# Performance work log

Measured on AMD Instinct MI355X. Metric: run time of the kernel, lower is better.

The kernel has to match this reference:

```python
import jax, jax.numpy as jnp
import numpy as np

STAGES = [80, 40, 20]
INPUT = 640
NUM_CLASSES = 80
B = 32
PRE_NMS = 1000      # top-k candidates fed to NMS (fixed-shape surrogate for full sort)
MAX_DET = 100       # max_num_detections
IOU_TH = 0.5
CLASS_OFF = 4096.0  # batched_nms trick: offset boxes per class so classes never overlap


def setup_inputs() -> dict:
    key = jax.random.key(0)
    ks = jax.random.split(key, 6)
    inp = {}
    for i, s in enumerate(STAGES):
        inp[f"cls{i}"] = jax.random.normal(ks[2 * i], (B, NUM_CLASSES, s, s), dtype=jnp.float32)
        # positive ltrb distances, up to ~64 px
        inp[f"box{i}"] = jax.random.uniform(ks[2 * i + 1], (B, 4, s, s), dtype=jnp.float32) * 64.0
    return inp


def _decode_level(cls, box, stage):
    # cls: [B,C,H,W], box: [B,4,H,W]
    step = INPUT // stage
    cls = jax.nn.sigmoid(jnp.transpose(cls, (0, 2, 3, 1)))   # [B,H,W,C]
    conf = jnp.max(cls, axis=-1)                             # [B,H,W]
    cidx = jnp.argmax(cls, axis=-1)                          # [B,H,W]
    box = jnp.transpose(box, (0, 2, 3, 1))                   # [B,H,W,4]
    grid = jnp.arange(stage, dtype=box.dtype) * step
    gx, gy = jnp.meshgrid(grid, grid, indexing='xy')
    block = jnp.stack([gx, gy], axis=-1)                     # [H,W,2]
    xy1 = block - box[..., :2]
    xy2 = block + box[..., 2:4]
    boxes = jnp.concatenate([xy1, xy2], axis=-1).reshape(box.shape[0], -1, 4)
    return boxes, conf.reshape(conf.shape[0], -1), cidx.reshape(cidx.shape[0], -1)


def _iou_matrix(b):
    # b: [N,4] -> [N,N] pairwise IoU
    area = jnp.maximum(b[:, 2] - b[:, 0], 0.) * jnp.maximum(b[:, 3] - b[:, 1], 0.)
    lt = jnp.maximum(b[:, None, :2], b[None, :, :2])
    rb = jnp.minimum(b[:, None, 2:], b[None, :, 2:])
    wh = jnp.maximum(rb - lt, 0.)
    inter = wh[..., 0] * wh[..., 1]
    return inter / (area[:, None] + area[None, :] - inter + 1e-7)


def _nms_image(boxes, scores, classes):
    # class-aware (batched) NMS via per-class coordinate offset
    off = classes.astype(boxes.dtype) * CLASS_OFF
    ob = boxes + off[:, None]
    s_top, idx = jax.lax.top_k(scores, PRE_NMS)
    b_top = ob[idx]                                          # [PRE,4], score-sorted desc
    iou = _iou_matrix(b_top)
    ar = jnp.arange(PRE_NMS)

    def body(i, supp):
        row = (iou[i] > IOU_TH) & (ar > i)
        return jnp.where(supp[i], supp, supp | row)

    supp = jax.lax.fori_loop(0, PRE_NMS, body, jnp.zeros((PRE_NMS,), bool))
    kept_scores = jnp.where(supp, -jnp.inf, s_top)
    sel_s, sel = jax.lax.top_k(kept_scores, MAX_DET)
    final = idx[sel]                                         # indices into original 8400
    valid = jnp.isfinite(sel_s)
    out_b = jnp.where(valid[:, None], boxes[final], 0.)
    out_s = jnp.where(valid, scores[final], 0.)
    out_c = jnp.where(valid, classes[final], -1)
    return out_b, out_s, out_c


def reference(cls0, box0, cls1, box1, cls2, box2):
    parts = [_decode_level(c, b, s) for c, b, s in
             zip([cls0, cls1, cls2], [box0, box1, box2], STAGES)]
    boxes = jnp.concatenate([p[0] for p in parts], axis=1)    # [B,8400,4]
    scores = jnp.concatenate([p[1] for p in parts], axis=1)   # [B,8400]
    classes = jnp.concatenate([p[2] for p in parts], axis=1)  # [B,8400]
    ob, os_, oc = jax.vmap(_nms_image)(boxes, scores, classes)
    boxes_with_scores = jnp.concatenate([ob, os_[..., None]], axis=-1)  # [B,MAX_DET,5]
    return boxes_with_scores, oc
```

## Files before the change

kernel.cpp:

```cpp
#include <hip/hip_runtime.h>

typedef unsigned int u32;
typedef unsigned long long u64;

#define NB 32
#define NCLS 80
#define NANCHOR 8400
#define PRE 1000
#define MAXDET 100
#define NT 1024

__global__ void decode_kernel(const float* __restrict__ cls0, const float* __restrict__ box0,
                              const float* __restrict__ cls1, const float* __restrict__ box1,
                              const float* __restrict__ cls2, const float* __restrict__ box2,
                              float* __restrict__ ws_scores, float4* __restrict__ ws_boxes,
                              int* __restrict__ ws_cls) {
    int g = blockIdx.x * blockDim.x + threadIdx.x;
    if (g >= NB * NANCHOR) return;
    int b = g / NANCHOR;
    int r = g - b * NANCHOR;

    const float* cp; const float* bp;
    int HW, hw, h, w, step;
    if (r < 6400) {
        cp = cls0 + (size_t)b * NCLS * 6400; bp = box0 + (size_t)b * 4 * 6400;
        HW = 6400; hw = r;        h = hw / 80; w = hw - h * 80; step = 8;
    } else if (r < 8000) {
        cp = cls1 + (size_t)b * NCLS * 1600; bp = box1 + (size_t)b * 4 * 1600;
        HW = 1600; hw = r - 6400; h = hw / 40; w = hw - h * 40; step = 16;
    } else {
        cp = cls2 + (size_t)b * NCLS * 400;  bp = box2 + (size_t)b * 4 * 400;
        HW = 400;  hw = r - 8000; h = hw / 20; w = hw - h * 20; step = 32;
    }

    float m = cp[hw];
    int ci = 0;
    for (int c = 1; c < NCLS; ++c) {
        float v = cp[(size_t)c * HW + hw];
        if (v > m) { m = v; ci = c; }
    }
    float score = 1.0f / (1.0f + expf(-m));

    float l = bp[hw], t = bp[HW + hw], rr = bp[2 * HW + hw], bo = bp[3 * HW + hw];
    float gx = (float)(w * step), gy = (float)(h * step);

    ws_scores[g] = score;
    ws_boxes[g] = make_float4(gx - l, gy - t, gx + rr, gy + bo);
    ws_cls[g] = ci;
}

__global__ __launch_bounds__(NT) void nms_kernel(const float* __restrict__ ws_scores,
                                                 const float4* __restrict__ ws_boxes,
                                                 const int* __restrict__ ws_cls,
                                                 float* __restrict__ out) {
    const int b = blockIdx.x;
    const int tid = threadIdx.x;

    __shared__ int s_hist[1024];
    __shared__ u64 s_key[2048];
    __shared__ float s_x1[PRE], s_y1[PRE], s_x2[PRE], s_y2[PRE], s_area[PRE];
    __shared__ int s_supp[PRE];
    __shared__ int s_keep[MAXDET];
    __shared__ int s_C, s_base;
    __shared__ u32 s_thresh;
    __shared__ int s_cnt;

    const float* sc = ws_scores + (size_t)b * NANCHOR;

    s_hist[tid] = 0;
    __syncthreads();
    for (int a = tid; a < NANCHOR; a += NT) {
        u32 sb = __float_as_uint(sc[a]);
        atomicAdd(&s_hist[sb >> 20], 1);
    }
    __syncthreads();
    for (int off = 1; off < 1024; off <<= 1) {
        int v = s_hist[tid];
        int u = (tid + off < 1024) ? s_hist[tid + off] : 0;
        __syncthreads();
        s_hist[tid] = v + u;
        __syncthreads();
    }
    {
        int sfx = s_hist[tid];
        int nxt = (tid < 1023) ? s_hist[tid + 1] : 0;
        if (sfx >= PRE && (tid == 1023 || nxt < PRE)) { s_C = tid; s_base = nxt; }
    }
    __syncthreads();
    const int C = s_C, base = s_base;
    __syncthreads();

    s_hist[tid] = 0;
    __syncthreads();
    for (int a = tid; a < NANCHOR; a += NT) {
        u32 sb = __float_as_uint(sc[a]);
        if ((int)(sb >> 20) == C) atomicAdd(&s_hist[(sb >> 10) & 1023], 1);
    }
    __syncthreads();
    for (int off = 1; off < 1024; off <<= 1) {
        int v = s_hist[tid];
        int u = (tid + off < 1024) ? s_hist[tid + off] : 0;
        __syncthreads();
        s_hist[tid] = v + u;
        __syncthreads();
    }
    {
        int sfx = base + s_hist[tid];
        int nxt = base + ((tid < 1023) ? s_hist[tid + 1] : 0);
        if (sfx >= PRE && (tid == 1023 || nxt < PRE))
            s_thresh = ((u32)C << 20) | ((u32)tid << 10);
    }
    if (tid == 0) s_cnt = 0;
    s_key[tid] = 0ULL;
    s_key[tid + 1024] = 0ULL;
    __syncthreads();
    const u32 thresh = s_thresh;

    for (int a = tid; a < NANCHOR; a += NT) {
        u32 sb = __float_as_uint(sc[a]);
        if (sb >= thresh) {
            int pos = atomicAdd(&s_cnt, 1);
            if (pos < 2048)
                s_key[pos] = ((u64)sb << 14) | (u64)(NANCHOR - 1 - a);
        }
    }
    __syncthreads();

    for (int k = 2; k <= 2048; k <<= 1) {
        for (int j = k >> 1; j > 0; j >>= 1) {
            for (int i = tid; i < 2048; i += NT) {
                int ixj = i ^ j;
                if (ixj > i) {
                    u64 va = s_key[i], vb = s_key[ixj];
                    bool desc = ((i & k) == 0);
                    if (desc ? (va < vb) : (va > vb)) { s_key[i] = vb; s_key[ixj] = va; }
                }
            }
            __syncthreads();
        }
    }

    if (tid < PRE) {
        u64 key = s_key[tid];
        int idx = (NANCHOR - 1) - (int)(key & 16383ULL);
        float4 bx = ws_boxes[(size_t)b * NANCHOR + idx];
        int c = ws_cls[(size_t)b * NANCHOR + idx];
        float off = (float)c * 4096.0f;
        float x1 = bx.x + off, y1 = bx.y + off, x2 = bx.z + off, y2 = bx.w + off;
        s_x1[tid] = x1; s_y1[tid] = y1; s_x2[tid] = x2; s_y2[tid] = y2;
        s_area[tid] = fmaxf(x2 - x1, 0.0f) * fmaxf(y2 - y1, 0.0f);
        s_supp[tid] = 0;
    }
    __syncthreads();

    int nkept = 0;
    for (int i = 0; i < PRE; ++i) {
        if (s_supp[i]) continue;
        if (tid == 0) s_keep[nkept] = i;
        nkept++;
        if (nkept >= MAXDET) break;
        float xi1 = s_x1[i], yi1 = s_y1[i], xi2 = s_x2[i], yi2 = s_y2[i], ai = s_area[i];
        int j = i + 1 + tid;
        if (j < PRE && !s_supp[j]) {
            float lx = fmaxf(xi1, s_x1[j]);
            float ly = fmaxf(yi1, s_y1[j]);
            float rx = fminf(xi2, s_x2[j]);
            float ry = fminf(yi2, s_y2[j]);
            float wx = fmaxf(rx - lx, 0.0f);
            float wy = fmaxf(ry - ly, 0.0f);
            float inter = wx * wy;
            float iou = inter / (ai + s_area[j] - inter + 1e-7f);
            if (iou > 0.5f) s_supp[j] = 1;
        }
        __syncthreads();
    }
    __syncthreads();

    if (tid < MAXDET) {
        float* o = out + ((size_t)b * MAXDET + tid) * 5;
        float* oc = out + (size_t)NB * MAXDET * 5 + (size_t)b * MAXDET + tid;
        if (tid < nkept) {
            int i = s_keep[tid];
            u64 key = s_key[i];
            int idx = (NANCHOR - 1) - (int)(key & 16383ULL);
            float score = __uint_as_float((u32)(key >> 14));
            float4 bx = ws_boxes[(size_t)b * NANCHOR + idx];
            int c = ws_cls[(size_t)b * NANCHOR + idx];
            o[0] = bx.x; o[1] = bx.y; o[2] = bx.z; o[3] = bx.w; o[4] = score;
            *oc = (float)c;
        } else {
            o[0] = 0.0f; o[1] = 0.0f; o[2] = 0.0f; o[3] = 0.0f; o[4] = 0.0f;
            *oc = -1.0f;
        }
    }
}

extern "C" void kernel_launch(void* const* d_in, const int* in_sizes, int n_in,
                              void* d_out, int out_size, void* d_ws, size_t ws_size,
                              hipStream_t stream) {
    const float* cls0 = (const float*)d_in[0];
    const float* box0 = (const float*)d_in[1];
    const float* cls1 = (const float*)d_in[2];
    const float* box1 = (const float*)d_in[3];
    const float* cls2 = (const float*)d_in[4];
    const float* box2 = (const float*)d_in[5];

    float* ws = (float*)d_ws;
    float* ws_scores = ws;
    float4* ws_boxes = (float4*)(ws + NB * NANCHOR);
    int* ws_cls = (int*)(ws + (size_t)NB * NANCHOR * 5);

    int total = NB * NANCHOR;
    decode_kernel<<<(total + 255) / 256, 256, 0, stream>>>(
        cls0, box0, cls1, box1, cls2, box2, ws_scores, ws_boxes, ws_cls);

    nms_kernel<<<NB, NT, 0, stream>>>(ws_scores, ws_boxes, ws_cls, (float*)d_out);
}
```

Before: 206.7 us.

## Split NMS into select/sort, parallel IoU bitmask, and wave-level scan kernels

Splits the single per-image NMS kernel into three kernels. A select/sort kernel caches scores in LDS, uses wave-shuffle suffix scans, and shrinks the bitonic sort to 1024 entries when possible, replacing small-stride barriers with wave barriers. An IoU kernel spread over 16 blocks per image builds a 64-bit suppression bitmask matrix, and a single-wavefront kernel walks that mask greedily using shuffles and readlane. The aim is to remove the serial loop that needed a block barrier per candidate and to parallelise IoU across many more CUs, at the cost of extra launches and workspace traffic.

```diff
diff --git a/kernel.cpp b/kernel.cpp
--- a/kernel.cpp
+++ b/kernel.cpp
@@ -49,38 +49,76 @@
     ws_cls[g] = ci;
 }
 
-__global__ __launch_bounds__(NT) void nms_kernel(const float* __restrict__ ws_scores,
-                                                 const float4* __restrict__ ws_boxes,
-                                                 const int* __restrict__ ws_cls,
-                                                 float* __restrict__ out) {
+__device__ __forceinline__ u64 shfl_xor_u64(u64 v, int m) {
+    u32 lo = (u32)v, hi = (u32)(v >> 32);
+    lo = (u32)__shfl_xor((int)lo, m, 64);
+    hi = (u32)__shfl_xor((int)hi, m, 64);
+    return ((u64)hi << 32) | (u64)lo;
+}
+
+__device__ __forceinline__ u64 readlane_u64(u64 v, int l) {
+    u32 lo = (u32)v, hi = (u32)(v >> 32);
+    lo = (u32)__builtin_amdgcn_readlane((int)lo, l);
+    hi = (u32)__builtin_amdgcn_readlane((int)hi, l);
+    return ((u64)hi << 32) | (u64)lo;
+}
+
+__device__ __forceinline__ void suffix_scan_1024(int* sh, int* swsum, int* swadd) {
+    const int tid = threadIdx.x, lane = tid & 63, wv = tid >> 6;
+    int s = sh[tid];
+#pragma unroll
+    for (int off = 1; off < 64; off <<= 1) {
+        int u = __shfl_down(s, off, 64);
+        if (lane + off < 64) s += u;
+    }
+    if (lane == 0) swsum[wv] = s;
+    __syncthreads();
+    if (tid < 64) {
+        int t = (lane < 16) ? swsum[lane] : 0;
+#pragma unroll
+        for (int off = 1; off < 16; off <<= 1) {
+            int u = __shfl_down(t, off, 64);
+            if (lane + off < 64) t += u;
+        }
+        int ab = __shfl_down(t, 1, 64);
+        if (lane < 16) swadd[lane] = (lane == 15) ? 0 : ab;
+    }
+    __syncthreads();
+    sh[tid] = s + swadd[wv];
+    __syncthreads();
+}
+
+__global__ __launch_bounds__(NT) void select_sort_kernel(
+        const float* __restrict__ ws_scores, const float4* __restrict__ ws_boxes,
+        const int* __restrict__ ws_cls, u64* __restrict__ ws_keys,
+        float* __restrict__ ws_sx1, float* __restrict__ ws_sy1,
+        float* __restrict__ ws_sx2, float* __restrict__ ws_sy2,
+        float* __restrict__ ws_sar) {
     const int b = blockIdx.x;
     const int tid = threadIdx.x;
 
+    __shared__ u32 s_sb[NANCHOR];
     __shared__ int s_hist[1024];
     __shared__ u64 s_key[2048];
-    __shared__ float s_x1[PRE], s_y1[PRE], s_x2[PRE], s_y2[PRE], s_area[PRE];
-    __shared__ int s_supp[PRE];
-    __shared__ int s_keep[MAXDET];
-    __shared__ int s_C, s_base;
+    __shared__ int s_wsum[16], s_wadd[16];
+    __shared__ int s_C, s_base, s_cnt;
     __shared__ u32 s_thresh;
-    __shared__ int s_cnt;
 
     const float* sc = ws_scores + (size_t)b * NANCHOR;
 
     s_hist[tid] = 0;
-    __syncthreads();
+    s_key[tid] = 0ULL;
+    s_key[tid + 1024] = 0ULL;
+    if (tid == 0) s_cnt = 0;
+    __syncthreads();
+
     for (int a = tid; a < NANCHOR; a += NT) {
         u32 sb = __float_as_uint(sc[a]);
+        s_sb[a] = sb;
         atomicAdd(&s_hist[sb >> 20], 1);
     }
     __syncthreads();
-    for (int off = 1; off < 1024; off <<= 1) {
-        int v = s_hist[tid];
-        int u = (tid + off < 1024) ? s_hist[tid + off] : 0;
-        __syncthreads();
-        s_hist[tid] = v + u;
-        __syncthreads();
-    }
+    suffix_scan_1024(s_hist, s_wsum, s_wadd);
     {
         int sfx = s_hist[tid];
         int nxt = (tid < 1023) ? s_hist[tid + 1] : 0;
@@ -88,36 +126,26 @@
     }
     __syncthreads();
     const int C = s_C, base = s_base;
-    __syncthreads();
-
     s_hist[tid] = 0;
     __syncthreads();
+
     for (int a = tid; a < NANCHOR; a += NT) {
-        u32 sb = __float_as_uint(sc[a]);
+        u32 sb = s_sb[a];
         if ((int)(sb >> 20) == C) atomicAdd(&s_hist[(sb >> 10) & 1023], 1);
     }
     __syncthreads();
-    for (int off = 1; off < 1024; off <<= 1) {
-        int v = s_hist[tid];
-        int u = (tid + off < 1024) ? s_hist[tid + off] : 0;
-        __syncthreads();
-        s_hist[tid] = v + u;
-        __syncthreads();
-    }
+    suffix_scan_1024(s_hist, s_wsum, s_wadd);
     {
         int sfx = base + s_hist[tid];
         int nxt = base + ((tid < 1023) ? s_hist[tid + 1] : 0);
         if (sfx >= PRE && (tid == 1023 || nxt < PRE))
             s_thresh = ((u32)C << 20) | ((u32)tid << 10);
     }
-    if (tid == 0) s_cnt = 0;
-    s_key[tid] = 0ULL;
-    s_key[tid + 1024] = 0ULL;
     __syncthreads();
     const u32 thresh = s_thresh;
 
     for (int a = tid; a < NANCHOR; a += NT) {
-        u32 sb = __float_as_uint(sc[a]);
+        u32 sb = s_sb[a];
         if (sb >= thresh) {
             int pos = atomicAdd(&s_cnt, 1);
             if (pos < 2048)
@@ -125,10 +153,16 @@
         }
     }
     __syncthreads();
-
-    for (int k = 2; k <= 2048; k <<= 1) {
+    const int cnt = s_cnt;
+    const int sortN = (cnt <= 1024) ? 1024 : 2048;
+
+    bool prevBig = false;
+    for (int k = 2; k <= sortN; k <<= 1) {
         for (int j = k >> 1; j > 0; j >>= 1) {
-            for (int i = tid; i < 2048; i += NT) {
+            const bool big = (j >= 64);
+            if (big || prevBig) __syncthreads();
+            else __builtin_amdgcn_wave_barrier();
+            for (int i = tid; i < sortN; i += NT) {
                 int ixj = i ^ j;
                 if (ixj > i) {
                     u64 va = s_key[i], vb = s_key[ixj];
@@ -136,52 +170,119 @@
                     if (desc ? (va < vb) : (va > vb)) { s_key[i] = vb; s_key[ixj] = va; }
                 }
             }
-            __syncthreads();
-        }
-    }
-
-    if (tid < PRE) {
+            prevBig = big;
+        }
+    }
+    __syncthreads();
+
+    {
         u64 key = s_key[tid];
+        ws_keys[(b << 10) + tid] = key;
         int idx = (NANCHOR - 1) - (int)(key & 16383ULL);
         float4 bx = ws_boxes[(size_t)b * NANCHOR + idx];
         int c = ws_cls[(size_t)b * NANCHOR + idx];
         float off = (float)c * 4096.0f;
         float x1 = bx.x + off, y1 = bx.y + off, x2 = bx.z + off, y2 = bx.w + off;
-        s_x1[tid] = x1; s_y1[tid] = y1; s_x2[tid] = x2; s_y2[tid] = y2;
-        s_area[tid] = fmaxf(x2 - x1, 0.0f) * fmaxf(y2 - y1, 0.0f);
-        s_supp[tid] = 0;
-    }
-    __syncthreads();
-
-    int nkept = 0;
-    for (int i = 0; i < PRE; ++i) {
-        if (s_supp[i]) continue;
-        if (tid == 0) s_keep[nkept] = i;
-        nkept++;
-        if (nkept >= MAXDET) break;
-        float xi1 = s_x1[i], yi1 = s_y1[i], xi2 = s_x2[i], yi2 = s_y2[i], ai = s_area[i];
-        int j = i + 1 + tid;
-        if (j < PRE && !s_supp[j]) {
-            float lx = fmaxf(xi1, s_x1[j]);
-            float ly = fmaxf(yi1, s_y1[j]);
-            float rx = fminf(xi2, s_x2[j]);
-            float ry = fminf(yi2, s_y2[j]);
+        int o = (b << 10) + tid;
+        ws_sx1[o] = x1; ws_sy1[o] = y1; ws_sx2[o] = x2; ws_sy2[o] = y2;
+        ws_sar[o] = fmaxf(x2 - x1, 0.0f) * fmaxf(y2 - y1, 0.0f);
+    }
+}
+
+__global__ __launch_bounds__(1024) void iou_bits_kernel(
+        const float* __restrict__ ws_sx1, const float* __restrict__ ws_sy1,
+        const float* __restrict__ ws_sx2, const float* __restrict__ ws_sy2,
+        const float* __restrict__ ws_sar,
+        u64* __restrict__ ws_bits, u64* __restrict__ ws_diag) {
+    const int blk = blockIdx.x;
+    const int b = blk >> 4, tile = blk & 15;
+    const int tid = threadIdx.x;
+
+    __shared__ float sx1[1024], sy1[1024], sx2[1024], sy2[1024], sar[1024];
+    {
+        int o = (b << 10) + tid;
+        sx1[tid] = ws_sx1[o]; sy1[tid] = ws_sy1[o];
+        sx2[tid] = ws_sx2[o]; sy2[tid] = ws_sy2[o];
+        sar[tid] = ws_sar[o];
+    }
+    __syncthreads();
+
+    const int rl = tid & 63, w = tid >> 6;
+    const int r = (tile << 6) + rl;
+    u64 bits = 0ULL;
+    if (r < 1000 && w >= tile) {
+        float xi1 = sx1[r], yi1 = sy1[r], xi2 = sx2[r], yi2 = sy2[r], ai = sar[r];
+        const int jbase = w << 6;
+#pragma unroll 8
+        for (int kb = 0; kb < 64; ++kb) {
+            int j = jbase + kb;
+            float lx = fmaxf(xi1, sx1[j]);
+            float ly = fmaxf(yi1, sy1[j]);
+            float rx = fminf(xi2, sx2[j]);
+            float ry = fminf(yi2, sy2[j]);
             float wx = fmaxf(rx - lx, 0.0f);
             float wy = fmaxf(ry - ly, 0.0f);
             float inter = wx * wy;
-            float iou = inter / (ai + s_area[j] - inter + 1e-7f);
-            if (iou > 0.5f) s_supp[j] = 1;
-        }
-        __syncthreads();
-    }
-    __syncthreads();
-
+            float iou = inter / (ai + sar[j] - inter + 1e-7f);
+            bits |= (iou > 0.5f) ? (1ULL << kb) : 0ULL;
+        }
+        u64 mlow;
+        if (w == tile) {
+            int bpos = r & 63;
+            mlow = (bpos == 63) ? 0ULL : (~0ULL << (bpos + 1));
+        } else mlow = ~0ULL;
+        u64 mhigh = (jbase + 64 <= 1000) ? ~0ULL : ((1ULL << (1000 - jbase)) - 1ULL);
+        bits &= mlow & mhigh;
+    }
+    ws_bits[((size_t)b << 14) + ((size_t)r << 4) + w] = bits;
+    if (w == tile) ws_diag[(b << 10) + r] = bits;
+}
+
+__global__ __launch_bounds__(128) void nms_scan_kernel(
+        const u64* __restrict__ ws_bits, const u64* __restrict__ ws_diag,
+        const u64* __restrict__ ws_keys, const float4* __restrict__ ws_boxes,
+        const int* __restrict__ ws_cls, float* __restrict__ out) {
+    const int b = blockIdx.x;
+    const int tid = threadIdx.x;
+
+    __shared__ int s_keep[MAXDET];
+    __shared__ int s_nk;
+
+    if (tid < 64) {
+        const int lane = tid;
+        const u64* bits = ws_bits + ((size_t)b << 14);
+        const u64* diag = ws_diag + ((size_t)b << 10);
+        int nkept = 0;
+        for (int wi = 0; wi < 16 && nkept < MAXDET; ++wi) {
+            const int wbase = wi << 6;
+            u64 acc = 0ULL;
+            if (lane < nkept)       acc  = bits[((size_t)s_keep[lane] << 4) + wi];
+            if (lane + 64 < nkept)  acc |= bits[((size_t)s_keep[lane + 64] << 4) + wi];
+#pragma unroll
+            for (int off = 32; off > 0; off >>= 1) acc |= shfl_xor_u64(acc, off);
+            u64 cur = acc;
+            u64 rw = diag[wbase + lane];
+            const int nb = (wbase + 64 <= 1000) ? 64 : (1000 - wbase);
+            for (int bit = 0; bit < nb; ++bit) {
+                if (!((cur >> bit) & 1ULL)) {
+                    if (lane == 0) s_keep[nkept] = wbase + bit;
+                    nkept++;
+                    if (nkept >= MAXDET) break;
+                    cur |= readlane_u64(rw, bit);
+                }
+            }
+        }
+        if (lane == 0) s_nk = nkept;
+    }
+    __syncthreads();
+
+    const int nk = s_nk;
     if (tid < MAXDET) {
         float* o = out + ((size_t)b * MAXDET + tid) * 5;
         float* oc = out + (size_t)NB * MAXDET * 5 + (size_t)b * MAXDET + tid;
-        if (tid < nkept) {
-            int i = s_keep[tid];
-            u64 key = s_key[i];
+        if (tid < nk) {
+            int rank = s_keep[tid];
+            u64 key = ws_keys[(b << 10) + rank];
             int idx = (NANCHOR - 1) - (int)(key & 16383ULL);
             float score = __uint_as_float((u32)(key >> 14));
             float4 bx = ws_boxes[(size_t)b * NANCHOR + idx];
@@ -209,10 +310,26 @@
     float* ws_scores = ws;
     float4* ws_boxes = (float4*)(ws + NB * NANCHOR);
     int* ws_cls = (int*)(ws + (size_t)NB * NANCHOR * 5);
+    float* base6 = ws + (size_t)NB * NANCHOR * 6;
+    u64* ws_keys = (u64*)base6;
+    float* ws_sx1 = base6 + 65536;
+    float* ws_sy1 = ws_sx1 + NB * 1024;
+    float* ws_sx2 = ws_sy1 + NB * 1024;
+    float* ws_sy2 = ws_sx2 + NB * 1024;
+    float* ws_sar = ws_sy2 + NB * 1024;
+    u64* ws_bits = (u64*)(ws_sar + NB * 1024);
+    u64* ws_diag = ws_bits + (size_t)NB * 1024 * 16;
 
     int total = NB * NANCHOR;
     decode_kernel<<<(total + 255) / 256, 256, 0, stream>>>(
         cls0, box0, cls1, box1, cls2, box2, ws_scores, ws_boxes, ws_cls);
 
-    nms_kernel<<<NB, NT, 0, stream>>>(ws_scores, ws_boxes, ws_cls, (float*)d_out);
-}
+    select_sort_kernel<<<NB, NT, 0, stream>>>(ws_scores, ws_boxes, ws_cls, ws_keys,
+                                              ws_sx1, ws_sy1, ws_sx2, ws_sy2, ws_sar);
+
+    iou_bits_kernel<<<NB * 16, 1024, 0, stream>>>(ws_sx1, ws_sy1, ws_sx2, ws_sy2, ws_sar,
+                                                  ws_bits, ws_diag);
+
+    nms_scan_kernel<<<NB, 128, 0, stream>>>(ws_bits, ws_diag, ws_keys, ws_boxes, ws_cls,
+                                            (float*)d_out);
+}
```

Result: faster. 187.0 us (-9.5%).
